# Optimization experiments

Hardware: AMD Instinct MI355X
Metric: run time of the kernel (lower is better)

Reference implementation:

```python
import jax, jax.numpy as jnp
import numpy as np
import itertools

N_ELEC = 128
BOX_L = 10.0
DIM = 3
BATCH = 4096


def gen_kpoints(N, L, dim):
    # Faithful numpy port of genKpoints (FermiNet make_kpoints variant).
    rec = 2.0 * np.pi / L
    dk = 1.0 + 1e-05
    max_k = int((N * dk) ** (1.0 / dim) + 0.5)
    ordinals = sorted(range(-max_k, max_k + 1), key=abs)
    ords = np.array(list(itertools.product(ordinals, repeat=dim)), dtype=np.float64)
    kpoints = ords * rec
    order = np.argsort(np.linalg.norm(kpoints, axis=1), kind='stable')
    kpoints = kpoints[order]
    return kpoints[:N].astype(np.float32)


def make_switches(kpoints, dim):
    # Select cos for k-points on the 'positive' side, sin(-k.r) for the rest.
    weights = 10.0 ** np.arange(1, dim + 1)
    weighted_sums = np.sign(kpoints).dot(weights)
    k_signs = np.sign(weighted_sums + 1.0)
    cos_switch = ((k_signs + 1.0) / 2.0).astype(np.float32)
    sin_switch = ((1.0 - k_signs) / 2.0).astype(np.float32)
    return cos_switch, sin_switch


def setup_inputs() -> dict:
    key = jax.random.key(0)
    rs = jax.random.uniform(key, (BATCH, N_ELEC, DIM), dtype=jnp.float32) * BOX_L
    kpoints = gen_kpoints(N_ELEC, BOX_L, DIM)
    cos_switch, sin_switch = make_switches(kpoints, DIM)
    return {
        'rs': rs,
        'kpoints': jnp.asarray(kpoints),
        'cos_switch': jnp.asarray(cos_switch),
        'sin_switch': jnp.asarray(sin_switch),
    }


def reference(rs, kpoints, cos_switch, sin_switch):
    # dots[b, i, m] = k_m . r_{b,i}   -> [B, N, N]
    dots = jnp.einsum('bnd,md->bnm', rs, kpoints)
    # Slater matrix: rows = particles, cols = plane-wave orbitals.
    slater = cos_switch * jnp.cos(dots) + sin_switch * jnp.sin(-dots)
    # log |det| per walker (batched LU) -> [B]
    return jnp.linalg.slogdet(slater)[1]
```

## Files before the change

kernel.cpp:

```cpp
#include <hip/hip_runtime.h>
#include <stdint.h>

#define NM 128
#define NT 512

typedef float v2f __attribute__((ext_vector_type(2)));

__device__ __forceinline__ float readlane_f(float v, int lane) {
    return __int_as_float(__builtin_amdgcn_readlane(__float_as_int(v), lane));
}

__device__ __forceinline__ unsigned wave_max_dpp(unsigned x) {
    int v = (int)x;
#define DPP_STEP(ctrl) \
    { int o = __builtin_amdgcn_update_dpp(0, v, ctrl, 0xf, 0xf, true); \
      v = ((unsigned)o > (unsigned)v) ? o : v; }
    DPP_STEP(0x111)
    DPP_STEP(0x112)
    DPP_STEP(0x114)
    DPP_STEP(0x118)
    DPP_STEP(0x142)
    DPP_STEP(0x143)
#undef DPP_STEP
    return (unsigned)v;
}

__device__ __forceinline__ unsigned pack_key(float v, int r) {
    return (((__float_as_uint(v) & 0x7fffffffu) >> 6) << 7) | (unsigned)r;
}

__device__ __forceinline__ unsigned argmax_bcast(unsigned ka, unsigned kb) {
    const unsigned m = wave_max_dpp(ka > kb ? ka : kb);
    return (unsigned)__builtin_amdgcn_readlane((int)m, 63);
}

__device__ __forceinline__ float sel_readlane(v2f c, int p) {
    return (p < 64) ? readlane_f(c.x, p) : readlane_f(c.y, p - 64);
}

template<int B>
__device__ __forceinline__ void extract_apply8(v2f (&sv)[16], int p, v2f lm) {
    float u[8];
    if (p < 64) {
#pragma unroll
        for (int j = 0; j < 8; ++j) u[j] = readlane_f(sv[B + j].x, p);
    } else {
#pragma unroll
        for (int j = 0; j < 8; ++j) u[j] = readlane_f(sv[B + j].y, p - 64);
    }
#pragma unroll
    for (int j = 0; j < 8; ++j)
        sv[B + j] = __builtin_elementwise_fma((v2f){-u[j], -u[j]}, lm, sv[B + j]);
}

template<int B>
__device__ __forceinline__ void lookahead8(v2f (&sv)[16], bool& elim0, bool& elim1,
                                           int r0, int r1, int l, int g,
                                           float2 (*colvg)[64],
                                           unsigned* keysF, float* pivsF,
                                           ulonglong2* masks) {
    const bool e0in = elim0, e1in = elim1;
#pragma unroll
    for (int i = 0; i < 8; ++i) {
        const v2f c = sv[B + i];
        const unsigned key = argmax_bcast(elim0 ? 0u : pack_key(c.x, r0),
                                          elim1 ? 0u : pack_key(c.y, r1));
        const int pu = __builtin_amdgcn_readfirstlane((int)(key & 127u));
        const float piv = sel_readlane(c, pu);
        const float rcp = __builtin_amdgcn_rcpf(piv);
        elim0 = elim0 || (r0 == pu);
        elim1 = elim1 || (r1 == pu);
        const v2f lm = { elim0 ? 0.0f : c.x * rcp,
                         elim1 ? 0.0f : c.y * rcp };
        colvg[i][l] = make_float2(lm.x, lm.y);
#pragma unroll
        for (int m = i + 1; m < 8; ++m) {
            const float u = sel_readlane(sv[B + m], pu);
            sv[B + m] = __builtin_elementwise_fma((v2f){-u, -u}, lm, sv[B + m]);
        }
        if (l == 0) { keysF[8 * g + i] = key; pivsF[8 * g + i] = piv; }
    }
    const unsigned long long b0 = __ballot(elim0 && !e0in);
    const unsigned long long b1 = __ballot(elim1 && !e1in);
    if (l == 0) masks[g] = make_ulonglong2(b0, b1);
}

__global__ __launch_bounds__(NT, 8)
void slater_logdet(const float* __restrict__ rs,
                   const float* __restrict__ kpts,
                   const float* __restrict__ csw,
                   const float* __restrict__ ssw,
                   float* __restrict__ out) {
    __shared__ float2 colv[2][8][64];
    __shared__ unsigned keysF[NM];
    __shared__ float    pivsF[NM];
    __shared__ ulonglong2 masks[NM / 8];
    __shared__ float    redf[2];

    const int t  = threadIdx.x;
    const int b  = blockIdx.x;
    const int w  = t >> 6;
    const int l  = t & 63;
    const int r0 = l, r1 = l + 64;

    v2f sv[16];
    {
        const float x0 = rs[(b * NM + r0) * 3 + 0];
        const float y0 = rs[(b * NM + r0) * 3 + 1];
        const float z0 = rs[(b * NM + r0) * 3 + 2];
        const float x1 = rs[(b * NM + r1) * 3 + 0];
        const float y1 = rs[(b * NM + r1) * 3 + 1];
        const float z1 = rs[(b * NM + r1) * 3 + 2];
#pragma unroll
        for (int j = 0; j < 16; ++j) {
            const int m = (j < 8) ? (8 * w + j) : (64 + 8 * w + (j - 8));
            const float kx = kpts[m * 3 + 0], ky = kpts[m * 3 + 1], kz = kpts[m * 3 + 2];
            const float cw = csw[m], sw = ssw[m];
            float sn, cn;
            __sincosf(kx * x0 + ky * y0 + kz * z0, &sn, &cn);
            sv[j].x = cw * cn - sw * sn;
            __sincosf(kx * x1 + ky * y1 + kz * z1, &sn, &cn);
            sv[j].y = cw * cn - sw * sn;
        }
    }

    bool elim0 = false, elim1 = false;

    if (w == 0)
        lookahead8<0>(sv, elim0, elim1, r0, r1, l, 0, colv[0], keysF, pivsF, masks);
    __syncthreads();

    const int liveEnd = w + 7;
    int rd = 0;
    for (; rd <= liveEnd; ++rd) {
        const uint4 ka = *(const uint4*)&keysF[8 * rd];
        const uint4 kb = *(const uint4*)&keysF[8 * rd + 4];
        int p[8];
        p[0] = __builtin_amdgcn_readfirstlane((int)(ka.x & 127u));
        p[1] = __builtin_amdgcn_readfirstlane((int)(ka.y & 127u));
        p[2] = __builtin_amdgcn_readfirstlane((int)(ka.z & 127u));
        p[3] = __builtin_amdgcn_readfirstlane((int)(ka.w & 127u));
        p[4] = __builtin_amdgcn_readfirstlane((int)(kb.x & 127u));
        p[5] = __builtin_amdgcn_readfirstlane((int)(kb.y & 127u));
        p[6] = __builtin_amdgcn_readfirstlane((int)(kb.z & 127u));
        p[7] = __builtin_amdgcn_readfirstlane((int)(kb.w & 127u));
        const ulonglong2 mk = masks[rd];
        elim0 = elim0 || (((mk.x >> l) & 1ull) != 0);
        elim1 = elim1 || (((mk.y >> l) & 1ull) != 0);

        const int par = rd & 1;
        if (rd < w) {
#pragma unroll
            for (int i = 0; i < 8; ++i) {
                const float2 la = colv[par][i][l];
                const v2f lm = (v2f){la.x, la.y};
                extract_apply8<0>(sv, p[i], lm);
                extract_apply8<8>(sv, p[i], lm);
            }
        } else {
#pragma unroll
            for (int i = 0; i < 8; ++i) {
                const float2 la = colv[par][i][l];
                extract_apply8<8>(sv, p[i], (v2f){la.x, la.y});
            }
        }

        if (rd == w - 1)
            lookahead8<0>(sv, elim0, elim1, r0, r1, l, rd + 1,
                          colv[(rd + 1) & 1], keysF, pivsF, masks);
        if (rd == w + 7)
            lookahead8<8>(sv, elim0, elim1, r0, r1, l, rd + 1,
                          colv[(rd + 1) & 1], keysF, pivsF, masks);

        __syncthreads();
    }
    for (; rd < 15; ++rd) __syncthreads();

    float lg = 0.0f;
    if (t < NM) {
        lg = __logf(fabsf(pivsF[t]));
#pragma unroll
        for (int off = 32; off > 0; off >>= 1)
            lg += __shfl_xor(lg, off, 64);
        if ((t & 63) == 0) redf[t >> 6] = lg;
    }
    __syncthreads();
    if (t == 0) out[b] = redf[0] + redf[1];
}

extern "C" void kernel_launch(void* const* d_in, const int* in_sizes, int n_in,
                              void* d_out, int out_size, void* d_ws, size_t ws_size,
                              hipStream_t stream) {
    const float* rs = (const float*)d_in[0];
    const float* kp = (const float*)d_in[1];
    const float* cs = (const float*)d_in[2];
    const float* ss = (const float*)d_in[3];
    float* out = (float*)d_out;
    const int batch = in_sizes[0] / (NM * 3);
    slater_logdet<<<dim3(batch), dim3(NT), 0, stream>>>(rs, kp, cs, ss, out);
}
```

Measured before the change: 372.1 us.

## Switch LU column distribution from interleaved 8-col panels to contiguous 16-col panels

Each wave now owns 16 contiguous columns instead of two 8-column groups at 8*w and 64+8*w, so the factorization runs as 8 panels of 16 rather than 16 panels of 8. This halves the number of block-wide barriers (7 rounds instead of 15) and removes the pipelined lookahead on the second half. In exchange, each panel factorization is serial and twice as long, and load balance worsens because later waves idle early while the last wave does the most work.

```diff
diff --git a/kernel.cpp b/kernel.cpp
--- a/kernel.cpp
+++ b/kernel.cpp
@@ -38,31 +38,15 @@
     return (p < 64) ? readlane_f(c.x, p) : readlane_f(c.y, p - 64);
 }
 
-template<int B>
-__device__ __forceinline__ void extract_apply8(v2f (&sv)[16], int p, v2f lm) {
-    float u[8];
-    if (p < 64) {
-#pragma unroll
-        for (int j = 0; j < 8; ++j) u[j] = readlane_f(sv[B + j].x, p);
-    } else {
-#pragma unroll
-        for (int j = 0; j < 8; ++j) u[j] = readlane_f(sv[B + j].y, p - 64);
-    }
-#pragma unroll
-    for (int j = 0; j < 8; ++j)
-        sv[B + j] = __builtin_elementwise_fma((v2f){-u[j], -u[j]}, lm, sv[B + j]);
-}
-
-template<int B>
-__device__ __forceinline__ void lookahead8(v2f (&sv)[16], bool& elim0, bool& elim1,
-                                           int r0, int r1, int l, int g,
-                                           float2 (*colvg)[64],
-                                           unsigned* keysF, float* pivsF,
-                                           ulonglong2* masks) {
+__device__ __forceinline__ void factor16(v2f (&sv)[16], bool& elim0, bool& elim1,
+                                         int r0, int r1, int l, int g,
+                                         float2 (*colvg)[64],
+                                         unsigned* keysF, float* pivsF,
+                                         ulonglong2* masks) {
     const bool e0in = elim0, e1in = elim1;
 #pragma unroll
-    for (int i = 0; i < 8; ++i) {
-        const v2f c = sv[B + i];
+    for (int i = 0; i < 16; ++i) {
+        const v2f c = sv[i];
         const unsigned key = argmax_bcast(elim0 ? 0u : pack_key(c.x, r0),
                                           elim1 ? 0u : pack_key(c.y, r1));
         const int pu = __builtin_amdgcn_readfirstlane((int)(key & 127u));
@@ -73,16 +57,57 @@
         const v2f lm = { elim0 ? 0.0f : c.x * rcp,
                          elim1 ? 0.0f : c.y * rcp };
         colvg[i][l] = make_float2(lm.x, lm.y);
+        float u[16];
+        if (pu < 64) {
 #pragma unroll
-        for (int m = i + 1; m < 8; ++m) {
-            const float u = sel_readlane(sv[B + m], pu);
-            sv[B + m] = __builtin_elementwise_fma((v2f){-u, -u}, lm, sv[B + m]);
+            for (int m = i + 1; m < 16; ++m) u[m] = readlane_f(sv[m].x, pu);
+        } else {
+#pragma unroll
+            for (int m = i + 1; m < 16; ++m) u[m] = readlane_f(sv[m].y, pu - 64);
         }
-        if (l == 0) { keysF[8 * g + i] = key; pivsF[8 * g + i] = piv; }
+#pragma unroll
+        for (int m = i + 1; m < 16; ++m)
+            sv[m] = __builtin_elementwise_fma((v2f){-u[m], -u[m]}, lm, sv[m]);
+        if (l == 0) { keysF[16 * g + i] = key; pivsF[16 * g + i] = piv; }
     }
     const unsigned long long b0 = __ballot(elim0 && !e0in);
     const unsigned long long b1 = __ballot(elim1 && !e1in);
     if (l == 0) masks[g] = make_ulonglong2(b0, b1);
+}
+
+template<int I0>
+__device__ __forceinline__ void apply8x16(v2f (&sv)[16],
+                                          const unsigned* keysR,
+                                          const float2 (*colvp)[64], int l) {
+    float2 la[8];
+#pragma unroll
+    for (int i = 0; i < 8; ++i) la[i] = colvp[I0 + i][l];
+    const uint4 ka = *(const uint4*)&keysR[I0];
+    const uint4 kb = *(const uint4*)&keysR[I0 + 4];
+    int p[8];
+    p[0] = __builtin_amdgcn_readfirstlane((int)(ka.x & 127u));
+    p[1] = __builtin_amdgcn_readfirstlane((int)(ka.y & 127u));
+    p[2] = __builtin_amdgcn_readfirstlane((int)(ka.z & 127u));
+    p[3] = __builtin_amdgcn_readfirstlane((int)(ka.w & 127u));
+    p[4] = __builtin_amdgcn_readfirstlane((int)(kb.x & 127u));
+    p[5] = __builtin_amdgcn_readfirstlane((int)(kb.y & 127u));
+    p[6] = __builtin_amdgcn_readfirstlane((int)(kb.z & 127u));
+    p[7] = __builtin_amdgcn_readfirstlane((int)(kb.w & 127u));
+#pragma unroll
+    for (int i = 0; i < 8; ++i) {
+        const v2f lm = (v2f){la[i].x, la[i].y};
+        float u[16];
+        if (p[i] < 64) {
+#pragma unroll
+            for (int j = 0; j < 16; ++j) u[j] = readlane_f(sv[j].x, p[i]);
+        } else {
+#pragma unroll
+            for (int j = 0; j < 16; ++j) u[j] = readlane_f(sv[j].y, p[i] - 64);
+        }
+#pragma unroll
+        for (int j = 0; j < 16; ++j)
+            sv[j] = __builtin_elementwise_fma((v2f){-u[j], -u[j]}, lm, sv[j]);
+    }
 }
 
 __global__ __launch_bounds__(NT, 8)
@@ -91,10 +116,10 @@
                    const float* __restrict__ csw,
                    const float* __restrict__ ssw,
                    float* __restrict__ out) {
-    __shared__ float2 colv[2][8][64];
+    __shared__ float2 colv[2][16][64];
     __shared__ unsigned keysF[NM];
     __shared__ float    pivsF[NM];
-    __shared__ ulonglong2 masks[NM / 8];
+    __shared__ ulonglong2 masks[NM / 16];
     __shared__ float    redf[2];
 
     const int t  = threadIdx.x;
@@ -113,7 +138,7 @@
         const float z1 = rs[(b * NM + r1) * 3 + 2];
 #pragma unroll
         for (int j = 0; j < 16; ++j) {
-            const int m = (j < 8) ? (8 * w + j) : (64 + 8 * w + (j - 8));
+            const int m = 16 * w + j;
             const float kx = kpts[m * 3 + 0], ky = kpts[m * 3 + 1], kz = kpts[m * 3 + 2];
             const float cw = csw[m], sw = ssw[m];
             float sn, cn;
@@ -127,54 +152,24 @@
     bool elim0 = false, elim1 = false;
 
     if (w == 0)
-        lookahead8<0>(sv, elim0, elim1, r0, r1, l, 0, colv[0], keysF, pivsF, masks);
+        factor16(sv, elim0, elim1, r0, r1, l, 0, colv[0], keysF, pivsF, masks);
     __syncthreads();
 
-    const int liveEnd = w + 7;
-    int rd = 0;
-    for (; rd <= liveEnd; ++rd) {
-        const uint4 ka = *(const uint4*)&keysF[8 * rd];
-        const uint4 kb = *(const uint4*)&keysF[8 * rd + 4];
-        int p[8];
-        p[0] = __builtin_amdgcn_readfirstlane((int)(ka.x & 127u));
-        p[1] = __builtin_amdgcn_readfirstlane((int)(ka.y & 127u));
-        p[2] = __builtin_amdgcn_readfirstlane((int)(ka.z & 127u));
-        p[3] = __builtin_amdgcn_readfirstlane((int)(ka.w & 127u));
-        p[4] = __builtin_amdgcn_readfirstlane((int)(kb.x & 127u));
-        p[5] = __builtin_amdgcn_readfirstlane((int)(kb.y & 127u));
-        p[6] = __builtin_amdgcn_readfirstlane((int)(kb.z & 127u));
-        p[7] = __builtin_amdgcn_readfirstlane((int)(kb.w & 127u));
-        const ulonglong2 mk = masks[rd];
-        elim0 = elim0 || (((mk.x >> l) & 1ull) != 0);
-        elim1 = elim1 || (((mk.y >> l) & 1ull) != 0);
-
-        const int par = rd & 1;
-        if (rd < w) {
-#pragma unroll
-            for (int i = 0; i < 8; ++i) {
-                const float2 la = colv[par][i][l];
-                const v2f lm = (v2f){la.x, la.y};
-                extract_apply8<0>(sv, p[i], lm);
-                extract_apply8<8>(sv, p[i], lm);
-            }
-        } else {
-#pragma unroll
-            for (int i = 0; i < 8; ++i) {
-                const float2 la = colv[par][i][l];
-                extract_apply8<8>(sv, p[i], (v2f){la.x, la.y});
-            }
+    for (int rd = 0; rd < 7; ++rd) {
+        if (w > rd) {
+            const ulonglong2 mk = masks[rd];
+            elim0 = elim0 || (((mk.x >> l) & 1ull) != 0);
+            elim1 = elim1 || (((mk.y >> l) & 1ull) != 0);
+            const unsigned* keysR = &keysF[16 * rd];
+            const float2 (*cp)[64] = colv[rd & 1];
+            apply8x16<0>(sv, keysR, cp, l);
+            apply8x16<8>(sv, keysR, cp, l);
+            if (w == rd + 1)
+                factor16(sv, elim0, elim1, r0, r1, l, rd + 1,
+                         colv[(rd + 1) & 1], keysF, pivsF, masks);
         }
-
-        if (rd == w - 1)
-            lookahead8<0>(sv, elim0, elim1, r0, r1, l, rd + 1,
-                          colv[(rd + 1) & 1], keysF, pivsF, masks);
-        if (rd == w + 7)
-            lookahead8<8>(sv, elim0, elim1, r0, r1, l, rd + 1,
-                          colv[(rd + 1) & 1], keysF, pivsF, masks);
-
         __syncthreads();
     }
-    for (; rd < 15; ++rd) __syncthreads();
 
     float lg = 0.0f;
     if (t < NM) {
```

New measurement: 457.1 us. 22.9% more time.

## Reverse high-column block assignment per wave to balance elimination work

Applied to the files above, without the earlier changes.

Wave w now owns column blocks w and 15-w instead of w and w+8, so each wave does a more even share of the trailing-update work and the last lookahead happens at round 14-w. The kernel also raises wave priority during the pivot-panel lookahead, and restructures the update loops to batch the readlane extractions before the FMAs. The aim is to shorten the critical path and the barrier waits caused by imbalanced waves. A leftover no-op conditional statement remains in the loop.

```diff
diff --git a/kernel.cpp b/kernel.cpp
--- a/kernel.cpp
+++ b/kernel.cpp
@@ -39,27 +39,13 @@
 }
 
 template<int B>
-__device__ __forceinline__ void extract_apply8(v2f (&sv)[16], int p, v2f lm) {
-    float u[8];
-    if (p < 64) {
-#pragma unroll
-        for (int j = 0; j < 8; ++j) u[j] = readlane_f(sv[B + j].x, p);
-    } else {
-#pragma unroll
-        for (int j = 0; j < 8; ++j) u[j] = readlane_f(sv[B + j].y, p - 64);
-    }
-#pragma unroll
-    for (int j = 0; j < 8; ++j)
-        sv[B + j] = __builtin_elementwise_fma((v2f){-u[j], -u[j]}, lm, sv[B + j]);
-}
-
-template<int B>
 __device__ __forceinline__ void lookahead8(v2f (&sv)[16], bool& elim0, bool& elim1,
                                            int r0, int r1, int l, int g,
                                            float2 (*colvg)[64],
                                            unsigned* keysF, float* pivsF,
                                            ulonglong2* masks) {
     const bool e0in = elim0, e1in = elim1;
+    __builtin_amdgcn_s_setprio(1);
 #pragma unroll
     for (int i = 0; i < 8; ++i) {
         const v2f c = sv[B + i];
@@ -73,16 +59,74 @@
         const v2f lm = { elim0 ? 0.0f : c.x * rcp,
                          elim1 ? 0.0f : c.y * rcp };
         colvg[i][l] = make_float2(lm.x, lm.y);
-#pragma unroll
-        for (int m = i + 1; m < 8; ++m) {
-            const float u = sel_readlane(sv[B + m], pu);
-            sv[B + m] = __builtin_elementwise_fma((v2f){-u, -u}, lm, sv[B + m]);
-        }
+        float u[8];
+        if (pu < 64) {
+#pragma unroll
+            for (int m = i + 1; m < 8; ++m) u[m] = readlane_f(sv[B + m].x, pu);
+        } else {
+#pragma unroll
+            for (int m = i + 1; m < 8; ++m) u[m] = readlane_f(sv[B + m].y, pu - 64);
+        }
+#pragma unroll
+        for (int m = i + 1; m < 8; ++m)
+            sv[B + m] = __builtin_elementwise_fma((v2f){-u[m], -u[m]}, lm, sv[B + m]);
         if (l == 0) { keysF[8 * g + i] = key; pivsF[8 * g + i] = piv; }
     }
+    __builtin_amdgcn_s_setprio(0);
     const unsigned long long b0 = __ballot(elim0 && !e0in);
     const unsigned long long b1 = __ballot(elim1 && !e1in);
     if (l == 0) masks[g] = make_ulonglong2(b0, b1);
+}
+
+__device__ __forceinline__ void decode_p(const unsigned* keysR, int (&p)[8]) {
+    const uint4 ka = *(const uint4*)&keysR[0];
+    const uint4 kb = *(const uint4*)&keysR[4];
+    p[0] = __builtin_amdgcn_readfirstlane((int)(ka.x & 127u));
+    p[1] = __builtin_amdgcn_readfirstlane((int)(ka.y & 127u));
+    p[2] = __builtin_amdgcn_readfirstlane((int)(ka.z & 127u));
+    p[3] = __builtin_amdgcn_readfirstlane((int)(ka.w & 127u));
+    p[4] = __builtin_amdgcn_readfirstlane((int)(kb.x & 127u));
+    p[5] = __builtin_amdgcn_readfirstlane((int)(kb.y & 127u));
+    p[6] = __builtin_amdgcn_readfirstlane((int)(kb.z & 127u));
+    p[7] = __builtin_amdgcn_readfirstlane((int)(kb.w & 127u));
+}
+
+__device__ __forceinline__ void apply16(v2f (&sv)[16], const int (&p)[8],
+                                        const float2 (&la)[8]) {
+#pragma unroll
+    for (int i = 0; i < 8; ++i) {
+        const v2f lm = (v2f){la[i].x, la[i].y};
+        float u[16];
+        if (p[i] < 64) {
+#pragma unroll
+            for (int j = 0; j < 16; ++j) u[j] = readlane_f(sv[j].x, p[i]);
+        } else {
+#pragma unroll
+            for (int j = 0; j < 16; ++j) u[j] = readlane_f(sv[j].y, p[i] - 64);
+        }
+#pragma unroll
+        for (int j = 0; j < 16; ++j)
+            sv[j] = __builtin_elementwise_fma((v2f){-u[j], -u[j]}, lm, sv[j]);
+    }
+}
+
+__device__ __forceinline__ void apply8hi(v2f (&sv)[16], const int (&p)[8],
+                                         const float2 (&la)[8]) {
+#pragma unroll
+    for (int i = 0; i < 8; ++i) {
+        const v2f lm = (v2f){la[i].x, la[i].y};
+        float u[8];
+        if (p[i] < 64) {
+#pragma unroll
+            for (int j = 0; j < 8; ++j) u[j] = readlane_f(sv[8 + j].x, p[i]);
+        } else {
+#pragma unroll
+            for (int j = 0; j < 8; ++j) u[j] = readlane_f(sv[8 + j].y, p[i] - 64);
+        }
+#pragma unroll
+        for (int j = 0; j < 8; ++j)
+            sv[8 + j] = __builtin_elementwise_fma((v2f){-u[j], -u[j]}, lm, sv[8 + j]);
+    }
 }
 
 __global__ __launch_bounds__(NT, 8)
@@ -113,7 +157,7 @@
         const float z1 = rs[(b * NM + r1) * 3 + 2];
 #pragma unroll
         for (int j = 0; j < 16; ++j) {
-            const int m = (j < 8) ? (8 * w + j) : (64 + 8 * w + (j - 8));
+            const int m = (j < 8) ? (8 * w + j) : (8 * (15 - w) + (j - 8));
             const float kx = kpts[m * 3 + 0], ky = kpts[m * 3 + 1], kz = kpts[m * 3 + 2];
             const float cw = csw[m], sw = ssw[m];
             float sn, cn;
@@ -130,45 +174,29 @@
         lookahead8<0>(sv, elim0, elim1, r0, r1, l, 0, colv[0], keysF, pivsF, masks);
     __syncthreads();
 
-    const int liveEnd = w + 7;
+    const int liveEnd = 14 - w;
     int rd = 0;
     for (; rd <= liveEnd; ++rd) {
-        const uint4 ka = *(const uint4*)&keysF[8 * rd];
-        const uint4 kb = *(const uint4*)&keysF[8 * rd + 4];
-        int p[8];
-        p[0] = __builtin_amdgcn_readfirstlane((int)(ka.x & 127u));
-        p[1] = __builtin_amdgcn_readfirstlane((int)(ka.y & 127u));
-        p[2] = __builtin_amdgcn_readfirstlane((int)(ka.z & 127u));
-        p[3] = __builtin_amdgcn_readfirstlane((int)(ka.w & 127u));
-        p[4] = __builtin_amdgcn_readfirstlane((int)(kb.x & 127u));
-        p[5] = __builtin_amdgcn_readfirstlane((int)(kb.y & 127u));
-        p[6] = __builtin_amdgcn_readfirstlane((int)(kb.z & 127u));
-        p[7] = __builtin_amdgcn_readfirstlane((int)(kb.w & 127u));
         const ulonglong2 mk = masks[rd];
         elim0 = elim0 || (((mk.x >> l) & 1ull) != 0);
         elim1 = elim1 || (((mk.y >> l) & 1ull) != 0);
 
-        const int par = rd & 1;
-        if (rd < w) {
-#pragma unroll
-            for (int i = 0; i < 8; ++i) {
-                const float2 la = colv[par][i][l];
-                const v2f lm = (v2f){la.x, la.y};
-                extract_apply8<0>(sv, p[i], lm);
-                extract_apply8<8>(sv, p[i], lm);
-            }
-        } else {
-#pragma unroll
-            for (int i = 0; i < 8; ++i) {
-                const float2 la = colv[par][i][l];
-                extract_apply8<8>(sv, p[i], (v2f){la.x, la.y});
-            }
-        }
+        int p[8];
+        decode_p(&keysF[8 * rd], p);
+        const float2 (*cp)[64] = colv[rd & 1];
+        float2 la[8];
+#pragma unroll
+        for (int i = 0; i < 8; ++i) la[i] = cp[i][l];
+
+        if (rd < w) apply16(sv, p, la);
+        else        apply8hi(sv, p, la);
 
         if (rd == w - 1)
             lookahead8<0>(sv, elim0, elim1, r0, r1, l, rd + 1,
                           colv[(rd + 1) & 1], keysF, pivsF, masks);
-        if (rd == w + 7)
+        if (rd == liveEnd && w != 0 + 0 ? (rd == 14 - w) : (rd == 14))
+            ;
+        if (rd == 14 - w)
             lookahead8<8>(sv, elim0, elim1, r0, r1, l, rd + 1,
                           colv[(rd + 1) & 1], keysF, pivsF, masks);
 
```

Result: slower. 423.4 us (+13.8%).
